# Kernel optimization log

Measured on AMD Instinct MI355X. Metric: run time of the kernel, lower is better.

The kernel has to match this reference:

```python
import jax, jax.numpy as jnp
import numpy as np
import math

N_SRC = 100000
N_DST0 = 30000
N_DST1 = 8000
E0 = 200000
E1 = 80000
H, D = 4, 64


def gat_conv(h_src, h_dst, src, dst, W, al, ar, b, n_dst):
    """DGL GATConv (allow_zero_in_degree=True): shared fc, LeakyReLU(0.2), edge softmax."""
    z_src = (h_src @ W).reshape(-1, H, D)              # [Ns,H,D]
    z_dst = (h_dst @ W).reshape(-1, H, D)              # [Nd,H,D]
    el = jnp.sum(z_src * al, axis=-1)                  # [Ns,H]
    er = jnp.sum(z_dst * ar, axis=-1)                  # [Nd,H]
    e = jax.nn.leaky_relu(el[src] + er[dst], 0.2)      # [E,H]
    emax = jax.ops.segment_max(e, dst, num_segments=n_dst)
    emax = jnp.where(jnp.isfinite(emax), emax, 0.0)
    ex = jnp.exp(e - emax[dst])
    denom = jax.ops.segment_sum(ex, dst, num_segments=n_dst)
    denom = jnp.where(denom > 0, denom, 1.0)
    alpha = ex / denom[dst]                            # [E,H]
    out = jax.ops.segment_sum(alpha[:, :, None] * z_src[src], dst, num_segments=n_dst)
    return out + b.reshape(1, H, D)                    # [Nd,H,D]


def attn_pool(feat):
    """Self attention over relation/head slots, then mean over slots (attention(f,f,f).mean(dim=1))."""
    d = feat.shape[-1]
    scores = jnp.einsum('nsd,ntd->nst', feat, feat) / math.sqrt(d)
    p = jax.nn.softmax(scores, axis=-1)
    out = jnp.einsum('nst,ntd->nsd', p, feat)
    return out.mean(axis=1)                            # [N,d]


def rgat_layer(xu, xi, eii, eiu, eui, W, al, ar, b, n_dst_u, n_dst_i):
    du, di = xu[:n_dst_u], xi[:n_dst_i]
    # sorted canonical etypes: ('item','ii','item') < ('item','iu','user') < ('user','ui','item')
    out_ii = gat_conv(xi, di, eii[0], eii[1], W[0], al[0], ar[0], b[0], n_dst_i)
    out_iu = gat_conv(xi, du, eiu[0], eiu[1], W[1], al[1], ar[1], b[1], n_dst_u)
    out_ui = gat_conv(xu, di, eui[0], eui[1], W[2], al[2], ar[2], b[2], n_dst_i)
    feat_u = out_iu                                    # [Nu, H, D]
    feat_i = jnp.concatenate([out_ii, out_ui], axis=1) # [Ni, 2H, D]
    hu = attn_pool(feat_u)
    hi = attn_pool(feat_i)
    return jnp.concatenate([du, hu], axis=1), jnp.concatenate([di, hi], axis=1)


def setup_inputs() -> dict:
    key = jax.random.key(0)
    ks = jax.random.split(key, 24)
    inp = {
        'x_user': jax.random.normal(ks[0], (N_SRC, 64), jnp.float32),
        'x_item': jax.random.normal(ks[1], (N_SRC, 64), jnp.float32),
        'e0_ii_src': jax.random.randint(ks[2], (E0,), 0, N_SRC, jnp.int32),
        'e0_ii_dst': jax.random.randint(ks[3], (E0,), 0, N_DST0, jnp.int32),
        'e0_iu_src': jax.random.randint(ks[4], (E0,), 0, N_SRC, jnp.int32),
        'e0_iu_dst': jax.random.randint(ks[5], (E0,), 0, N_DST0, jnp.int32),
        'e0_ui_src': jax.random.randint(ks[6], (E0,), 0, N_SRC, jnp.int32),
        'e0_ui_dst': jax.random.randint(ks[7], (E0,), 0, N_DST0, jnp.int32),
        'e1_ii_src': jax.random.randint(ks[8], (E1,), 0, N_DST0, jnp.int32),
        'e1_ii_dst': jax.random.randint(ks[9], (E1,), 0, N_DST1, jnp.int32),
        'e1_iu_src': jax.random.randint(ks[10], (E1,), 0, N_DST0, jnp.int32),
        'e1_iu_dst': jax.random.randint(ks[11], (E1,), 0, N_DST1, jnp.int32),
        'e1_ui_src': jax.random.randint(ks[12], (E1,), 0, N_DST0, jnp.int32),
        'e1_ui_dst': jax.random.randint(ks[13], (E1,), 0, N_DST1, jnp.int32),
        'W0': jax.random.normal(ks[14], (3, 64, H * D), jnp.float32) * 0.1,
        'al0': jax.random.normal(ks[15], (3, H, D), jnp.float32) * 0.1,
        'ar0': jax.random.normal(ks[16], (3, H, D), jnp.float32) * 0.1,
        'b0': jnp.zeros((3, H * D), jnp.float32),
        'W1': jax.random.normal(ks[17], (3, 128, H * D), jnp.float32) * 0.1,
        'al1': jax.random.normal(ks[18], (3, H, D), jnp.float32) * 0.1,
        'ar1': jax.random.normal(ks[19], (3, H, D), jnp.float32) * 0.1,
        'b1': jnp.zeros((3, H * D), jnp.float32),
    }
    return inp


def reference(x_user, x_item,
              e0_ii_src, e0_ii_dst, e0_iu_src, e0_iu_dst, e0_ui_src, e0_ui_dst,
              e1_ii_src, e1_ii_dst, e1_iu_src, e1_iu_dst, e1_ui_src, e1_ui_dst,
              W0, al0, ar0, b0, W1, al1, ar1, b1):
    xu, xi = rgat_layer(x_user, x_item,
                        (e0_ii_src, e0_ii_dst), (e0_iu_src, e0_iu_dst), (e0_ui_src, e0_ui_dst),
                        W0, al0, ar0, b0, N_DST0, N_DST0)
    xu, xi = rgat_layer(xu, xi,
                        (e1_ii_src, e1_ii_dst), (e1_iu_src, e1_iu_dst), (e1_ui_src, e1_ui_dst),
                        W1, al1, ar1, b1, N_DST1, N_DST1)
    return jnp.concatenate([xu, xi], axis=0)  # [2*N_DST1, 128+64]
```

## Files before the change

### kernel.cpp

```cpp
#include <hip/hip_runtime.h>

#define NSRC   100000
#define NDST0  30000
#define NDST1  8000
#define E0N    200000
#define E1N    80000
#define HD     256
#define DD     64
#define CAPB   32

typedef short bf16x8 __attribute__((ext_vector_type(8)));
typedef float f32x4  __attribute__((ext_vector_type(4)));

static __device__ __forceinline__ unsigned short f2bf(float f) {
    unsigned u = __float_as_uint(f);
    u += 0x7fffu + ((u >> 16) & 1u);
    return (unsigned short)(u >> 16);
}
static __device__ __forceinline__ unsigned pack2(float a, float b) {
    return (unsigned)f2bf(a) | ((unsigned)f2bf(b) << 16);
}
static __device__ __forceinline__ void fma4(float4& a, float s, const float4& b) {
    a.x = fmaf(s, b.x, a.x); a.y = fmaf(s, b.y, a.y);
    a.z = fmaf(s, b.z, a.z); a.w = fmaf(s, b.w, a.w);
}
static __device__ __forceinline__ float dot4(const float4& a, const float4& b) {
    return fmaf(a.x, b.x, fmaf(a.y, b.y, fmaf(a.z, b.z, a.w * b.w)));
}
static __device__ __forceinline__ float4 ld_bf4(const unsigned short* p) {
    uint2 u = *reinterpret_cast<const uint2*>(p);
    float4 r;
    r.x = __uint_as_float(u.x << 16);
    r.y = __uint_as_float(u.x & 0xffff0000u);
    r.z = __uint_as_float(u.y << 16);
    r.w = __uint_as_float(u.y & 0xffff0000u);
    return r;
}

static __device__ void wlr_prep(const float* __restrict__ W, const float* __restrict__ al,
                                const float* __restrict__ ar, float* __restrict__ wl,
                                float* __restrict__ wr, int K, int tid)
{
    int r = tid / (K * 4);
    int rem = tid - r * K * 4;
    int k = rem >> 2, h = rem & 3;
    const float* wrow = W + (size_t)r * K * HD + (size_t)k * HD + h * DD;
    const float* a_l = al + r * HD + h * DD;
    const float* a_r = ar + r * HD + h * DD;
    float sl = 0.f, sr = 0.f;
    for (int d = 0; d < DD; ++d) {
        float w = wrow[d];
        sl = fmaf(w, a_l[d], sl);
        sr = fmaf(w, a_r[d], sr);
    }
    wl[r * 512 + k * 4 + h] = sl;
    wr[r * 512 + k * 4 + h] = sr;
}
static __device__ void wt_prep(const float* __restrict__ W, unsigned short* __restrict__ Wt,
                               int K, int r, int c)
{
    const float* Wr = W + (size_t)r * K * HD;
    unsigned short* Wtr = Wt + (size_t)r * 256 * K;
    for (int k = 0; k < K; k += 2) {
        float a = Wr[(size_t)k * HD + c];
        float b = Wr[(size_t)(k + 1) * HD + c];
        *reinterpret_cast<unsigned*>(Wtr + (size_t)c * K + k) = pack2(a, b);
    }
}
static __device__ void fill_aos(const int* __restrict__ ed, const int* __restrict__ es,
                                int* __restrict__ cnt, int* __restrict__ bsrc,
                                int E, int nd, int r, int e)
{
    if (e >= E) return;
    int d = ed[e];
    int c = atomicAdd(&cnt[(size_t)r * nd + d], 1);
    if (c < CAPB) bsrc[((size_t)r * nd + d) * CAPB + c] = es[e];
}
template<int K>
static __device__ void prep_row(bool item, int row, int nd,
                                const float* __restrict__ XA, const float* __restrict__ XB,
                                const float* __restrict__ wl3, const float* __restrict__ wr3,
                                float* __restrict__ el3, float* __restrict__ er3)
{
    const float* X = item ? XA : XB;
    const float4* xv = reinterpret_cast<const float4*>(X + (size_t)row * K);
    const float4* wlAv = reinterpret_cast<const float4*>(item ? wl3 : wl3 + 1024);
    const float4* wlBv = reinterpret_cast<const float4*>(wl3 + 512);
    float4 aA = make_float4(0.f, 0.f, 0.f, 0.f), aB = aA;
    #pragma unroll
    for (int c = 0; c < K / 4; ++c) {
        float4 x4 = xv[c];
        fma4(aA, x4.x, wlAv[c * 4 + 0]); fma4(aA, x4.y, wlAv[c * 4 + 1]);
        fma4(aA, x4.z, wlAv[c * 4 + 2]); fma4(aA, x4.w, wlAv[c * 4 + 3]);
        if (item) {
            fma4(aB, x4.x, wlBv[c * 4 + 0]); fma4(aB, x4.y, wlBv[c * 4 + 1]);
            fma4(aB, x4.z, wlBv[c * 4 + 2]); fma4(aB, x4.w, wlBv[c * 4 + 3]);
        }
    }
    if (item) {
        *reinterpret_cast<float4*>(el3 + (size_t)row * 4) = aA;
        *reinterpret_cast<float4*>(el3 + (size_t)NSRC * 4 + (size_t)row * 4) = aB;
    } else {
        *reinterpret_cast<float4*>(el3 + (size_t)2 * NSRC * 4 + (size_t)row * 4) = aA;
    }
    if (row < nd) {
        const float4* wrAv = reinterpret_cast<const float4*>(item ? wr3 : wr3 + 512);
        const float4* wrBv = reinterpret_cast<const float4*>(wr3 + 1024);
        float4 rA = make_float4(0.f, 0.f, 0.f, 0.f), rB = rA;
        #pragma unroll
        for (int c = 0; c < K / 4; ++c) {
            float4 x4 = xv[c];
            fma4(rA, x4.x, wrAv[c * 4 + 0]); fma4(rA, x4.y, wrAv[c * 4 + 1]);
            fma4(rA, x4.z, wrAv[c * 4 + 2]); fma4(rA, x4.w, wrAv[c * 4 + 3]);
            if (item) {
                fma4(rB, x4.x, wrBv[c * 4 + 0]); fma4(rB, x4.y, wrBv[c * 4 + 1]);
                fma4(rB, x4.z, wrBv[c * 4 + 2]); fma4(rB, x4.w, wrBv[c * 4 + 3]);
            }
        }
        if (item) {
            *reinterpret_cast<float4*>(er3 + (size_t)row * 4) = rA;
            *reinterpret_cast<float4*>(er3 + (size_t)2 * NDST0 * 4 + (size_t)row * 4) = rB;
        } else {
            *reinterpret_cast<float4*>(er3 + (size_t)NDST0 * 4 + (size_t)row * 4) = rA;
        }
    }
}
template<int S>
static __device__ void pool_node(const unsigned short* __restrict__ srcA, const float* __restrict__ bA,
                                 const unsigned short* __restrict__ srcB, const float* __restrict__ bB,
                                 const float* __restrict__ base, int baseCols,
                                 float* __restrict__ dst, int pitch, int colOff,
                                 int node, int q)
{
    float4 f[S];
    #pragma unroll
    for (int s = 0; s < S; ++s) {
        const unsigned short* sp = (s < 4) ? (srcA + (size_t)node * HD + s * DD)
                                           : (srcB + (size_t)node * HD + (s - 4) * DD);
        const float* bp = (s < 4) ? (bA + s * DD) : (bB + (s - 4) * DD);
        float4 v = ld_bf4(sp + q * 4);
        float4 b = *reinterpret_cast<const float4*>(bp + q * 4);
        v.x += b.x; v.y += b.y; v.z += b.z; v.w += b.w;
        f[s] = v;
    }
    constexpr int NE = S * (S + 1) / 2;
    float gt[NE];
    {
        int idx = 0;
        #pragma unroll
        for (int s = 0; s < S; ++s)
            #pragma unroll
            for (int t = s; t < S; ++t)
                gt[idx++] = dot4(f[s], f[t]);
    }
    #pragma unroll
    for (int m = 1; m < 16; m <<= 1) {
        #pragma unroll
        for (int i = 0; i < NE; ++i) gt[i] += __shfl_xor(gt[i], m, 16);
    }
    auto Gv = [&](int s, int t) -> float {
        int a = s < t ? s : t, b2 = s < t ? t : s;
        return gt[a * S - a * (a - 1) / 2 + (b2 - a)];
    };
    float g[S];
    #pragma unroll
    for (int t = 0; t < S; ++t) g[t] = 0.f;
    #pragma unroll
    for (int s = 0; s < S; ++s) {
        float sc[S];
        float m = -1e30f;
        #pragma unroll
        for (int t = 0; t < S; ++t) { sc[t] = Gv(s, t) * 0.125f; m = sc[t] > m ? sc[t] : m; }
        float pe[S];
        float sum = 0.f;
        #pragma unroll
        for (int t = 0; t < S; ++t) { pe[t] = __expf(sc[t] - m); sum += pe[t]; }
        float inv = 1.f / sum;
        #pragma unroll
        for (int t = 0; t < S; ++t) g[t] += pe[t] * inv;
    }
    float4 o = make_float4(0.f, 0.f, 0.f, 0.f);
    #pragma unroll
    for (int t = 0; t < S; ++t) fma4(o, g[t], f[t]);
    const float is = 1.f / S;
    o.x *= is; o.y *= is; o.z *= is; o.w *= is;
    *reinterpret_cast<float4*>(dst + (size_t)node * pitch + colOff + q * 4) = o;
    for (int c = q * 4; c < baseCols; c += 64) {
        float4 v = *reinterpret_cast<const float4*>(base + (size_t)node * baseCols + c);
        *reinterpret_cast<float4*>(dst + (size_t)node * pitch + c) = v;
    }
}

__global__ __launch_bounds__(256) void k_setup(
    const int* ed0, const int* ed1, const int* ed2,
    const int* es0, const int* es1, const int* es2,
    int* cntA, int* bsrcA,
    const float* W0, const float* al0, const float* ar0,
    const float* W1, const float* al1, const float* ar1,
    float* wlA, float* wrA, unsigned short* WtA,
    float* wlB, float* wrB, unsigned short* WtB,
    int bpr0)
{
    int bx = blockIdx.x;
    int t = threadIdx.x;
    if (bx < 3 * bpr0) {
        int r = (bx >= 2 * bpr0) ? 2 : (bx >= bpr0 ? 1 : 0);
        int e = (bx - r * bpr0) * 256 + t;
        const int* ed = (r == 0) ? ed0 : (r == 1 ? ed1 : ed2);
        const int* es = (r == 0) ? es0 : (r == 1 ? es1 : es2);
        fill_aos(ed, es, cntA, bsrcA, E0N, NDST0, r, e);
        return;
    }
    bx -= 3 * bpr0;
    if (bx < 3)       wlr_prep(W0, al0, ar0, wlA, wrA, 64,  bx * 256 + t);
    else if (bx < 9)  wlr_prep(W1, al1, ar1, wlB, wrB, 128, (bx - 3) * 256 + t);
    else if (bx < 12) wt_prep(W0, WtA, 64,  bx - 9,  t);
    else              wt_prep(W1, WtB, 128, bx - 12, t);
}

template<int K>
__global__ __launch_bounds__(256) void k_prep_x2(const float* __restrict__ XA,
                                                 const float* __restrict__ XB,
                                                 int M, int nd, int bpr,
                                                 const float* __restrict__ wl3,
                                                 const float* __restrict__ wr3,
                                                 float* __restrict__ el3,
                                                 float* __restrict__ er3)
{
    int bx = blockIdx.x;
    const bool item = bx < bpr;
    int row = (item ? bx : bx - bpr) * 256 + threadIdx.x;
    if (row >= M) return;
    prep_row<K>(item, row, nd, XA, XB, wl3, wr3, el3, er3);
}

template<int K>
__global__ __launch_bounds__(256) void k_agg3(const int* __restrict__ cnt,
                                              const int* __restrict__ bsrc,
                                              const float* __restrict__ el3,
                                              const float* __restrict__ er3,
                                              const float* __restrict__ xsA,
                                              const float* __restrict__ xsB,
                                              unsigned short* __restrict__ aggX,
                                              int nd, int bpr)
{
    constexpr int NV = K / 64;
    __shared__ float exs[4][64][8];
    int bx = blockIdx.x;
    int r = (bx >= 2 * bpr) ? 2 : (bx >= bpr ? 1 : 0);
    int wid = ((bx - r * bpr) * 256 + (int)threadIdx.x) >> 6;
    int lane = threadIdx.x & 63;
    if (wid >= nd) return;
    int q = lane & 15, g = lane >> 4, w = threadIdx.x >> 6;
    const float* el = el3 + (size_t)r * NSRC * 4;
    const float* xsrc = (r < 2) ? xsA : xsB;
    int c = cnt[(size_t)r * nd + wid]; if (c > CAPB) c = CAPB;
    const int* lst = bsrc + ((size_t)r * nd + wid) * CAPB;
    float4 er4 = *reinterpret_cast<const float4*>(er3 + (size_t)r * NDST0 * 4 + (size_t)wid * 4);

    if (lane < c) {
        int s = lst[lane];
        float4 e4 = *reinterpret_cast<const float4*>(el + (size_t)s * 4);
        e4.x += er4.x; e4.y += er4.y; e4.z += er4.z; e4.w += er4.w;
        e4.x = e4.x > 0.f ? e4.x : 0.2f * e4.x;
        e4.y = e4.y > 0.f ? e4.y : 0.2f * e4.y;
        e4.z = e4.z > 0.f ? e4.z : 0.2f * e4.z;
        e4.w = e4.w > 0.f ? e4.w : 0.2f * e4.w;
        float sF = __int_as_float(s);
        float4 h0 = make_float4(sF, __expf(e4.x), sF, __expf(e4.y));
        float4 h1 = make_float4(sF, __expf(e4.z), sF, __expf(e4.w));
        *reinterpret_cast<float4*>(&exs[w][lane][0]) = h0;
        *reinterpret_cast<float4*>(&exs[w][lane][4]) = h1;
    }

    float4 acc[NV];
    #pragma unroll
    for (int v = 0; v < NV; ++v) acc[v] = make_float4(0.f, 0.f, 0.f, 0.f);
    float den = 0.f;
    const char* xb = reinterpret_cast<const char*>(xsrc) + q * (NV * 16);

    #pragma unroll 2
    for (int t = 0; t < c; ++t) {
        float2 se = *reinterpret_cast<const float2*>(&exs[w][t][g * 2]);
        int s = __float_as_int(se.x);
        float ex = se.y;
        const float4* xp = reinterpret_cast<const float4*>(xb + (size_t)((unsigned)s * (K * 4)));
        #pragma unroll
        for (int v = 0; v < NV; ++v) fma4(acc[v], ex, xp[v]);
        den += ex;
    }
    float inv = den > 0.f ? 1.f / den : 0.f;
    unsigned short* op = aggX + (((size_t)r * nd + wid) * 4 + g) * K + q * 4 * NV;
    if (NV == 1) {
        uint2 wv;
        wv.x = pack2(acc[0].x * inv, acc[0].y * inv);
        wv.y = pack2(acc[0].z * inv, acc[0].w * inv);
        *reinterpret_cast<uint2*>(op) = wv;
    } else {
        uint4 wv;
        wv.x = pack2(acc[0].x * inv, acc[0].y * inv);
        wv.y = pack2(acc[0].z * inv, acc[0].w * inv);
        wv.z = pack2(acc[1].x * inv, acc[1].y * inv);
        wv.w = pack2(acc[1].z * inv, acc[1].w * inv);
        *reinterpret_cast<uint4*>(op) = wv;
    }
}

template<int K>
__global__ __launch_bounds__(256) void k_gemm3(const unsigned short* __restrict__ aggX,
                                               const unsigned short* __restrict__ Wt3,
                                               unsigned short* __restrict__ outb,
                                               int nd, int bpr)
{
    int bx = blockIdx.x;
    int r = (bx >= 2 * bpr) ? 2 : (bx >= bpr ? 1 : 0);
    const unsigned short* A  = aggX + (size_t)r * nd * 4 * K;
    const unsigned short* Wt = Wt3 + (size_t)r * 256 * K;
    unsigned short* ob = outb + (size_t)r * NDST0 * HD;
    const int lane = threadIdx.x & 63;
    const int wv = threadIdx.x >> 6;
    const int r0 = (bx - r * bpr) * 16;
    const int rr = lane & 15, kg = lane >> 4;
    f32x4 acc[4] = {{0.f,0.f,0.f,0.f},{0.f,0.f,0.f,0.f},{0.f,0.f,0.f,0.f},{0.f,0.f,0.f,0.f}};
    const unsigned short* ap = A + ((size_t)(r0 + rr) * 4 + wv) * K + kg * 8;
    #pragma unroll
    for (int kb = 0; kb < K; kb += 32) {
        bf16x8 a = *reinterpret_cast<const bf16x8*>(ap + kb);
        #pragma unroll
        for (int n = 0; n < 4; ++n) {
            const unsigned short* wp = Wt + (size_t)(wv * 64 + n * 16 + rr) * K + kb + kg * 8;
            bf16x8 b = *reinterpret_cast<const bf16x8*>(wp);
            acc[n] = __builtin_amdgcn_mfma_f32_16x16x32_bf16(a, b, acc[n], 0, 0, 0);
        }
    }
    #pragma unroll
    for (int n = 0; n < 4; ++n)
        #pragma unroll
        for (int i = 0; i < 4; ++i)
            ob[(size_t)(r0 + kg * 4 + i) * HD + wv * 64 + n * 16 + rr] = f2bf(acc[n][i]);
}

__global__ __launch_bounds__(256) void k_pools(
    const unsigned short* pA4, const float* bA4, const unsigned short* pB4, const float* bB4,
    const float* base4, int cols4, float* dst4, int pitch4, int off4,
    const unsigned short* pA8, const float* bA8, const unsigned short* pB8, const float* bB8,
    const float* base8, int cols8, float* dst8, int pitch8, int off8,
    int n, int bp,
    const int* ed0, const int* ed1, const int* ed2,
    const int* es0, const int* es1, const int* es2,
    int* cnt, int* bsrc, int E, int nd, int bprF)
{
    int bx = blockIdx.x;
    int t = threadIdx.x;
    if (bx < 2 * bp) {
        const bool four = bx < bp;
        int bl = four ? bx : bx - bp;
        int node = ((bl * 256 + t) >> 6) * 4 + ((t & 63) >> 4);
        int q = t & 15;
        if (node >= n) return;
        if (four) pool_node<4>(pA4, bA4, pB4, bB4, base4, cols4, dst4, pitch4, off4, node, q);
        else      pool_node<8>(pA8, bA8, pB8, bB8, base8, cols8, dst8, pitch8, off8, node, q);
        return;
    }
    bx -= 2 * bp;
    int r = (bx >= 2 * bprF) ? 2 : (bx >= bprF ? 1 : 0);
    int e = (bx - r * bprF) * 256 + t;
    const int* ed = (r == 0) ? ed0 : (r == 1 ? ed1 : ed2);
    const int* es = (r == 0) ? es0 : (r == 1 ? es1 : es2);
    fill_aos(ed, es, cnt, bsrc, E, nd, r, e);
}

extern "C" void kernel_launch(void* const* d_in, const int* in_sizes, int n_in,
                              void* d_out, int out_size, void* d_ws, size_t ws_size,
                              hipStream_t stream)
{
    const float* x_user = (const float*)d_in[0];
    const float* x_item = (const float*)d_in[1];
    const int* e_s[6] = { (const int*)d_in[2], (const int*)d_in[4], (const int*)d_in[6],
                          (const int*)d_in[8], (const int*)d_in[10], (const int*)d_in[12] };
    const int* e_d[6] = { (const int*)d_in[3], (const int*)d_in[5], (const int*)d_in[7],
                          (const int*)d_in[9], (const int*)d_in[11], (const int*)d_in[13] };
    const float* W0  = (const float*)d_in[14];
    const float* al0 = (const float*)d_in[15];
    const float* ar0 = (const float*)d_in[16];
    const float* b0  = (const float*)d_in[17];
    const float* W1  = (const float*)d_in[18];
    const float* al1 = (const float*)d_in[19];
    const float* ar1 = (const float*)d_in[20];
    const float* b1  = (const float*)d_in[21];
    float* out = (float*)d_out;
    (void)in_sizes; (void)n_in; (void)out_size; (void)ws_size;

    char* p = (char*)d_ws;
    auto take = [&](size_t bytes) { char* r = p; p += (bytes + 255) & ~(size_t)255; return r; };
    unsigned short* out3 = (unsigned short*)take((size_t)3 * NDST0 * HD * 2);
    float* xu1  = (float*)take((size_t)NDST0 * 128 * 4);
    float* xi1  = (float*)take((size_t)NDST0 * 128 * 4);
    unsigned short* aggX = (unsigned short*)take((size_t)3 * NDST0 * 4 * DD * 2);
    float* el3  = (float*)take((size_t)3 * NSRC * 4 * 4);
    float* er3  = (float*)take((size_t)3 * NDST0 * 4 * 4);
    int*   cntA = (int*)take((size_t)3 * NDST0 * 4);
    int*   cntB = (int*)take((size_t)3 * NDST1 * 4);
    int*   bsrcA = (int*)take((size_t)3 * NDST0 * CAPB * 4);
    int*   bsrcB = (int*)take((size_t)3 * NDST1 * CAPB * 4);
    unsigned short* WtA = (unsigned short*)take((size_t)3 * 256 * 64 * 2);
    unsigned short* WtB = (unsigned short*)take((size_t)3 * 256 * 128 * 2);
    float* wlA = (float*)take((size_t)3 * 512 * 4);
    float* wrA = (float*)take((size_t)3 * 512 * 4);
    float* wlB = (float*)take((size_t)3 * 512 * 4);
    float* wrB = (float*)take((size_t)3 * 512 * 4);

    unsigned short* out_ii = out3;
    unsigned short* out_iu = out3 + (size_t)NDST0 * HD;
    unsigned short* out_ui = out3 + (size_t)2 * NDST0 * HD;

    {
        size_t cntSpan = (size_t)((char*)cntB - (char*)cntA) + (size_t)3 * NDST1 * 4;
        hipMemsetAsync(cntA, 0, cntSpan, stream);
    }
    const int bpr0 = (E0N + 255) / 256;
    k_setup<<<3 * bpr0 + 15, 256, 0, stream>>>(
        e_d[0], e_d[1], e_d[2], e_s[0], e_s[1], e_s[2],
        cntA, bsrcA,
        W0, al0, ar0, W1, al1, ar1,
        wlA, wrA, WtA, wlB, wrB, WtB, bpr0);

    {
        const int bprP = (NSRC + 255) / 256;
        k_prep_x2<64><<<2 * bprP, 256, 0, stream>>>(x_item, x_user, NSRC, NDST0, bprP,
                                                    wlA, wrA, el3, er3);
        const int bprA = (NDST0 + 3) / 4;
        k_agg3<64><<<3 * bprA, 256, 0, stream>>>(cntA, bsrcA, el3, er3, x_item, x_user,
                                                 aggX, NDST0, bprA);
        const int bprG = NDST0 / 16;
        k_gemm3<64><<<3 * bprG, 256, 0, stream>>>(aggX, WtA, out3, NDST0, bprG);
    }
    {
        const int bp = NDST0 / 16;
        const int bprF = (E1N + 255) / 256;
        k_pools<<<2 * bp + 3 * bprF, 256, 0, stream>>>(
            out_iu, b0 + 256, out_iu, b0 + 256, x_user, 64, xu1, 128, 64,
            out_ii, b0,       out_ui, b0 + 512, x_item, 64, xi1, 128, 64,
            NDST0, bp,
            e_d[3], e_d[4], e_d[5], e_s[3], e_s[4], e_s[5],
            cntB, bsrcB, E1N, NDST1, bprF);
    }

    {
        const int bprP = (NDST0 + 255) / 256;
        k_prep_x2<128><<<2 * bprP, 256, 0, stream>>>(xi1, xu1, NDST0, NDST1, bprP,
                                                     wlB, wrB, el3, er3);
        const int bprA = (NDST1 + 3) / 4;
        k_agg3<128><<<3 * bprA, 256, 0, stream>>>(cntB, bsrcB, el3, er3, xi1, xu1,
                                                  aggX, NDST1, bprA);
        const int bprG = NDST1 / 16;
        k_gemm3<128><<<3 * bprG, 256, 0, stream>>>(aggX, WtB, out3, NDST1, bprG);
    }
    {
        const int bp = NDST1 / 16;
        k_pools<<<2 * bp, 256, 0, stream>>>(
            out_iu, b1 + 256, out_iu, b1 + 256, xu1, 128, out, 192, 128,
            out_ii, b1,       out_ui, b1 + 512, xi1, 128, out + (size_t)NDST1 * 192, 192, 128,
            NDST1, bp,
            nullptr, nullptr, nullptr, nullptr, nullptr, nullptr,
            nullptr, nullptr, 0, 0, 0);
    }
}
```

Baseline: 295.1 us.

## Reschedule setup work across kernels and batch gathers in edge aggregation

Result: no change. 292.3 us (-0.9%).

```diff
diff --git a/kernel.cpp b/kernel.cpp
--- a/kernel.cpp
+++ b/kernel.cpp
@@ -191,18 +191,39 @@
     }
 }
 
-__global__ __launch_bounds__(256) void k_setup(
+__global__ void k_wsetup(const float* W0, const float* al0, const float* ar0,
+                         const float* W1, const float* al1, const float* ar1,
+                         float* wlA, float* wrA, unsigned short* WtA,
+                         float* wlB, float* wrB, unsigned short* WtB)
+{
+    int bx = blockIdx.x, t = threadIdx.x;
+    if (bx < 3)       wlr_prep(W0, al0, ar0, wlA, wrA, 64,  bx * 256 + t);
+    else if (bx < 9)  wlr_prep(W1, al1, ar1, wlB, wrB, 128, (bx - 3) * 256 + t);
+    else if (bx < 12) wt_prep(W0, WtA, 64,  bx - 9,  t);
+    else              wt_prep(W1, WtB, 128, bx - 12, t);
+}
+
+__global__ __launch_bounds__(256) void k_prepfill(
+    const float* x_item, const float* x_user,
+    const float* wlA, const float* wrA,
+    float* el3, float* er3,
     const int* ed0, const int* ed1, const int* ed2,
     const int* es0, const int* es1, const int* es2,
-    int* cntA, int* bsrcA,
-    const float* W0, const float* al0, const float* ar0,
-    const float* W1, const float* al1, const float* ar1,
-    float* wlA, float* wrA, unsigned short* WtA,
-    float* wlB, float* wrB, unsigned short* WtB,
-    int bpr0)
+    const int* ed3, const int* ed4, const int* ed5,
+    const int* es3, const int* es4, const int* es5,
+    int* cntA, int* bsrcA, int* cntB, int* bsrcB,
+    int bprP, int bpr0, int bpr1)
 {
     int bx = blockIdx.x;
     int t = threadIdx.x;
+    if (bx < 2 * bprP) {
+        const bool item = bx < bprP;
+        int row = (item ? bx : bx - bprP) * 256 + t;
+        if (row < NSRC)
+            prep_row<64>(item, row, NDST0, x_item, x_user, wlA, wrA, el3, er3);
+        return;
+    }
+    bx -= 2 * bprP;
     if (bx < 3 * bpr0) {
         int r = (bx >= 2 * bpr0) ? 2 : (bx >= bpr0 ? 1 : 0);
         int e = (bx - r * bpr0) * 256 + t;
@@ -212,10 +233,13 @@
         return;
     }
     bx -= 3 * bpr0;
-    if (bx < 3)       wlr_prep(W0, al0, ar0, wlA, wrA, 64,  bx * 256 + t);
-    else if (bx < 9)  wlr_prep(W1, al1, ar1, wlB, wrB, 128, (bx - 3) * 256 + t);
-    else if (bx < 12) wt_prep(W0, WtA, 64,  bx - 9,  t);
-    else              wt_prep(W1, WtB, 128, bx - 12, t);
+    {
+        int r = (bx >= 2 * bpr1) ? 2 : (bx >= bpr1 ? 1 : 0);
+        int e = (bx - r * bpr1) * 256 + t;
+        const int* ed = (r == 0) ? ed3 : (r == 1 ? ed4 : ed5);
+        const int* es = (r == 0) ? es3 : (r == 1 ? es4 : es5);
+        fill_aos(ed, es, cntB, bsrcB, E1N, NDST1, r, e);
+    }
 }
 
 template<int K>
@@ -279,15 +303,56 @@
     float den = 0.f;
     const char* xb = reinterpret_cast<const char*>(xsrc) + q * (NV * 16);
 
-    #pragma unroll 2
-    for (int t = 0; t < c; ++t) {
-        float2 se = *reinterpret_cast<const float2*>(&exs[w][t][g * 2]);
-        int s = __float_as_int(se.x);
-        float ex = se.y;
-        const float4* xp = reinterpret_cast<const float4*>(xb + (size_t)((unsigned)s * (K * 4)));
-        #pragma unroll
-        for (int v = 0; v < NV; ++v) fma4(acc[v], ex, xp[v]);
-        den += ex;
+    for (int b0 = 0; b0 < c; b0 += 4) {
+        const int n = c - b0;
+        float2 se0, se1, se2, se3;
+        float4 x0[NV], x1[NV], x2[NV], x3[NV];
+        se0 = *reinterpret_cast<const float2*>(&exs[w][b0][g * 2]);
+        {
+            const float4* xp = reinterpret_cast<const float4*>(
+                xb + (size_t)((unsigned)__float_as_int(se0.x) * (K * 4)));
+            #pragma unroll
+            for (int v = 0; v < NV; ++v) x0[v] = xp[v];
+        }
+        if (n > 1) {
+            se1 = *reinterpret_cast<const float2*>(&exs[w][b0 + 1][g * 2]);
+            const float4* xp = reinterpret_cast<const float4*>(
+                xb + (size_t)((unsigned)__float_as_int(se1.x) * (K * 4)));
+            #pragma unroll
+            for (int v = 0; v < NV; ++v) x1[v] = xp[v];
+        }
+        if (n > 2) {
+            se2 = *reinterpret_cast<const float2*>(&exs[w][b0 + 2][g * 2]);
+            const float4* xp = reinterpret_cast<const float4*>(
+                xb + (size_t)((unsigned)__float_as_int(se2.x) * (K * 4)));
+            #pragma unroll
+            for (int v = 0; v < NV; ++v) x2[v] = xp[v];
+        }
+        if (n > 3) {
+            se3 = *reinterpret_cast<const float2*>(&exs[w][b0 + 3][g * 2]);
+            const float4* xp = reinterpret_cast<const float4*>(
+                xb + (size_t)((unsigned)__float_as_int(se3.x) * (K * 4)));
+            #pragma unroll
+            for (int v = 0; v < NV; ++v) x3[v] = xp[v];
+        }
+        den += se0.y;
+        #pragma unroll
+        for (int v = 0; v < NV; ++v) fma4(acc[v], se0.y, x0[v]);
+        if (n > 1) {
+            den += se1.y;
+            #pragma unroll
+            for (int v = 0; v < NV; ++v) fma4(acc[v], se1.y, x1[v]);
+        }
+        if (n > 2) {
+            den += se2.y;
+            #pragma unroll
+            for (int v = 0; v < NV; ++v) fma4(acc[v], se2.y, x2[v]);
+        }
+        if (n > 3) {
+            den += se3.y;
+            #pragma unroll
+            for (int v = 0; v < NV; ++v) fma4(acc[v], se3.y, x3[v]);
+        }
     }
     float inv = den > 0.f ? 1.f / den : 0.f;
     unsigned short* op = aggX + (((size_t)r * nd + wid) * 4 + g) * K + q * 4 * NV;
@@ -345,29 +410,17 @@
     const float* base4, int cols4, float* dst4, int pitch4, int off4,
     const unsigned short* pA8, const float* bA8, const unsigned short* pB8, const float* bB8,
     const float* base8, int cols8, float* dst8, int pitch8, int off8,
-    int n, int bp,
-    const int* ed0, const int* ed1, const int* ed2,
-    const int* es0, const int* es1, const int* es2,
-    int* cnt, int* bsrc, int E, int nd, int bprF)
+    int n, int bp)
 {
     int bx = blockIdx.x;
     int t = threadIdx.x;
-    if (bx < 2 * bp) {
-        const bool four = bx < bp;
-        int bl = four ? bx : bx - bp;
-        int node = ((bl * 256 + t) >> 6) * 4 + ((t & 63) >> 4);
-        int q = t & 15;
-        if (node >= n) return;
-        if (four) pool_node<4>(pA4, bA4, pB4, bB4, base4, cols4, dst4, pitch4, off4, node, q);
-        else      pool_node<8>(pA8, bA8, pB8, bB8, base8, cols8, dst8, pitch8, off8, node, q);
-        return;
-    }
-    bx -= 2 * bp;
-    int r = (bx >= 2 * bprF) ? 2 : (bx >= bprF ? 1 : 0);
-    int e = (bx - r * bprF) * 256 + t;
-    const int* ed = (r == 0) ? ed0 : (r == 1 ? ed1 : ed2);
-    const int* es = (r == 0) ? es0 : (r == 1 ? es1 : es2);
-    fill_aos(ed, es, cnt, bsrc, E, nd, r, e);
+    const bool four = bx < bp;
+    int bl = four ? bx : bx - bp;
+    int node = ((bl * 256 + t) >> 6) * 4 + ((t & 63) >> 4);
+    int q = t & 15;
+    if (node >= n) return;
+    if (four) pool_node<4>(pA4, bA4, pB4, bB4, base4, cols4, dst4, pitch4, off4, node, q);
+    else      pool_node<8>(pA8, bA8, pB8, bB8, base8, cols8, dst8, pitch8, off8, node, q);
 }
 
 extern "C" void kernel_launch(void* const* d_in, const int* in_sizes, int n_in,
@@ -418,51 +471,43 @@
         size_t cntSpan = (size_t)((char*)cntB - (char*)cntA) + (size_t)3 * NDST1 * 4;
         hipMemsetAsync(cntA, 0, cntSpan, stream);
     }
+    k_wsetup<<<15, 256, 0, stream>>>(W0, al0, ar0, W1, al1, ar1,
+                                     wlA, wrA, WtA, wlB, wrB, WtB);
+    const int bprP = (NSRC + 255) / 256;
     const int bpr0 = (E0N + 255) / 256;
-    k_setup<<<3 * bpr0 + 15, 256, 0, stream>>>(
+    const int bpr1 = (E1N + 255) / 256;
+    k_prepfill<<<2 * bprP + 3 * bpr0 + 3 * bpr1, 256, 0, stream>>>(
+        x_item, x_user, wlA, wrA, el3, er3,
         e_d[0], e_d[1], e_d[2], e_s[0], e_s[1], e_s[2],
-        cntA, bsrcA,
-        W0, al0, ar0, W1, al1, ar1,
-        wlA, wrA, WtA, wlB, wrB, WtB, bpr0);
+        e_d[3], e_d[4], e_d[5], e_s[3], e_s[4], e_s[5],
+        cntA, bsrcA, cntB, bsrcB, bprP, bpr0, bpr1);
 
     {
-        const int bprP = (NSRC + 255) / 256;
-        k_prep_x2<64><<<2 * bprP, 256, 0, stream>>>(x_item, x_user, NSRC, NDST0, bprP,
-                                                    wlA, wrA, el3, er3);
         const int bprA = (NDST0 + 3) / 4;
         k_agg3<64><<<3 * bprA, 256, 0, stream>>>(cntA, bsrcA, el3, er3, x_item, x_user,
                                                  aggX, NDST0, bprA);
         const int bprG = NDST0 / 16;
         k_gemm3<64><<<3 * bprG, 256, 0, stream>>>(aggX, WtA, out3, NDST0, bprG);
-    }
-    {
         const int bp = NDST0 / 16;
-        const int bprF = (E1N + 255) / 256;
-        k_pools<<<2 * bp + 3 * bprF, 256, 0, stream>>>(
+        k_pools<<<2 * bp, 256, 0, stream>>>(
             out_iu, b0 + 256, out_iu, b0 + 256, x_user, 64, xu1, 128, 64,
             out_ii, b0,       out_ui, b0 + 512, x_item, 64, xi1, 128, 64,
-            NDST0, bp,
-            e_d[3], e_d[4], e_d[5], e_s[3], e_s[4], e_s[5],
-            cntB, bsrcB, E1N, NDST1, bprF);
+            NDST0, bp);
     }
 
     {
-        const int bprP = (NDST0 + 255) / 256;
-        k_prep_x2<128><<<2 * bprP, 256, 0, stream>>>(xi1, xu1, NDST0, NDST1, bprP,
-                                                     wlB, wrB, el3, er3);
+        const int bprP2 = (NDST0 + 255) / 256;
+        k_prep_x2<128><<<2 * bprP2, 256, 0, stream>>>(xi1, xu1, NDST0, NDST1, bprP2,
+                                                      wlB, wrB, el3, er3);
         const int bprA = (NDST1 + 3) / 4;
         k_agg3<128><<<3 * bprA, 256, 0, stream>>>(cntB, bsrcB, el3, er3, xi1, xu1,
                                                   aggX, NDST1, bprA);
         const int bprG = NDST1 / 16;
         k_gemm3<128><<<3 * bprG, 256, 0, stream>>>(aggX, WtB, out3, NDST1, bprG);
-    }
-    {
         const int bp = NDST1 / 16;
         k_pools<<<2 * bp, 256, 0, stream>>>(
             out_iu, b1 + 256, out_iu, b1 + 256, xu1, 128, out, 192, 128,
             out_ii, b1,       out_ui, b1 + 512, xi1, 128, out + (size_t)NDST1 * 192, 192, 128,
-            NDST1, bp,
-            nullptr, nullptr, nullptr, nullptr, nullptr, nullptr,
-            nullptr, nullptr, 0, 0, 0);
-    }
-}
+            NDST1, bp);
+    }
+}
```
